# Performance work log

Measured on AMD Instinct MI355X. Metric: run time of the kernel, lower is better.

The kernel has to match this reference:

```python
import jax, jax.numpy as jnp
import numpy as np
import math

DIM = 1024
HEADS = 16
HEAD_DIM = DIM // HEADS
FFN = 4096
B, S = 2, 2048
EPS = 1e-12


def layernorm(x, w, b):
    u = jnp.mean(x, axis=-1, keepdims=True)
    s = jnp.mean((x - u) ** 2, axis=-1, keepdims=True)
    return w * ((x - u) / jnp.sqrt(s + EPS)) + b


def setup_inputs() -> dict:
    key = jax.random.key(0)
    ks = jax.random.split(key, 8)
    scale = 0.02
    return {
        "x": jax.random.normal(ks[0], (B, S, DIM), dtype=jnp.float32),
        "mask": jnp.zeros((1, 1, S, S), dtype=jnp.float32),
        "wq": jax.random.normal(ks[1], (DIM, DIM), dtype=jnp.float32) * scale,
        "wk": jax.random.normal(ks[2], (DIM, DIM), dtype=jnp.float32) * scale,
        "wv": jax.random.normal(ks[3], (DIM, DIM), dtype=jnp.float32) * scale,
        "wo": jax.random.normal(ks[4], (DIM, DIM), dtype=jnp.float32) * scale,
        "w1": jax.random.normal(ks[5], (DIM, FFN), dtype=jnp.float32) * scale,
        "w2": jax.random.normal(ks[6], (FFN, DIM), dtype=jnp.float32) * scale,
        "ln1_w": jnp.ones((DIM,), dtype=jnp.float32),
        "ln1_b": jnp.zeros((DIM,), dtype=jnp.float32),
        "ln2_w": jnp.ones((DIM,), dtype=jnp.float32),
        "ln2_b": jnp.zeros((DIM,), dtype=jnp.float32),
    }


def reference(x, mask, wq, wk, wv, wo, w1, w2, ln1_w, ln1_b, ln2_w, ln2_b):
    # --- attention sub-block (pre-LN) ---
    h = layernorm(x, ln1_w, ln1_b)
    q = (h @ wq).reshape(B, S, HEADS, HEAD_DIM).transpose(0, 2, 1, 3)  # [B,H,S,D]
    k = (h @ wk).reshape(B, S, HEADS, HEAD_DIM).transpose(0, 2, 1, 3)
    v = (h @ wv).reshape(B, S, HEADS, HEAD_DIM).transpose(0, 2, 1, 3)
    scores = jnp.einsum("bhsd,bhtd->bhst", q, k) / math.sqrt(HEAD_DIM)
    scores = scores + mask
    probs = jax.nn.softmax(scores.astype(jnp.float32), axis=-1).astype(q.dtype)
    attn = jnp.einsum("bhst,bhtd->bhsd", probs, v)  # [B,H,S,D]
    attn = attn.transpose(0, 2, 1, 3).reshape(B, S, DIM)
    x = x + attn @ wo
    # --- FFN sub-block (pre-LN) ---
    h = layernorm(x, ln2_w, ln2_b)
    m = jax.nn.gelu(h @ w1, approximate=False) @ w2
    return x + m
```

## Files before the change

kernel.cpp:

```cpp
#include <hip/hip_runtime.h>
#include <math.h>


#define DIMSZ 1024
#define SEQ   2048
#define BATCH 2
#define NHEAD 16
#define HD    64
#define FFNSZ 4096
#define ROWS  (BATCH*SEQ)

typedef __attribute__((ext_vector_type(8))) short bf8_t;
typedef __attribute__((ext_vector_type(4))) float f4_t;

__device__ __forceinline__ unsigned short f2bf(float f) {
  union { float f; unsigned u; } c; c.f = f;
  unsigned u = c.u;
  return (unsigned short)((u + 0x7fffu + ((u >> 16) & 1u)) >> 16);
}

__device__ __forceinline__ float fast_exp2(float x) {
#if __has_builtin(__builtin_amdgcn_exp2f)
  return __builtin_amdgcn_exp2f(x);
#else
  return exp2f(x);
#endif
}

__device__ __forceinline__ unsigned int pk_trunc_bf16(float a, float b) {
#if __has_builtin(__builtin_amdgcn_perm)
  return __builtin_amdgcn_perm(__float_as_uint(b), __float_as_uint(a), 0x07060302u);
#else
  return (__float_as_uint(b) & 0xffff0000u) | (__float_as_uint(a) >> 16);
#endif
}

__device__ __forceinline__ void async16(const void* g, void* l) {
  __builtin_amdgcn_global_load_lds((const __attribute__((address_space(1))) void*)g,
                                   (__attribute__((address_space(3))) void*)l,
                                   16, 0, 0);
}

__device__ __forceinline__ f4_t mfma_bf16(bf8_t a, bf8_t b, f4_t c) {
  return __builtin_amdgcn_mfma_f32_16x16x32_bf16(a, b, c, 0, 0, 0);
}

__global__ __launch_bounds__(256) void ln_kernel(const float* __restrict__ x,
                                                 const float* __restrict__ w,
                                                 const float* __restrict__ b,
                                                 unsigned short* __restrict__ out) {
  int row  = blockIdx.x * 4 + (threadIdx.x >> 6);
  int lane = threadIdx.x & 63;
  const float4* xr = (const float4*)(x + (size_t)row * DIMSZ);
  float4 v[4];
  float s = 0.f, s2 = 0.f;
#pragma unroll
  for (int i = 0; i < 4; ++i) {
    v[i] = xr[lane + 64*i];
    s  += (v[i].x + v[i].y) + (v[i].z + v[i].w);
    s2 += (v[i].x*v[i].x + v[i].y*v[i].y) + (v[i].z*v[i].z + v[i].w*v[i].w);
  }
#pragma unroll
  for (int off = 32; off; off >>= 1) {
    s  += __shfl_xor(s,  off);
    s2 += __shfl_xor(s2, off);
  }
  float mean = s * (1.f/DIMSZ);
  float var  = s2 * (1.f/DIMSZ) - mean*mean;
  float rstd = rsqrtf(var + 1e-12f);
  const float4* wr = (const float4*)w;
  const float4* br = (const float4*)b;
#pragma unroll
  for (int i = 0; i < 4; ++i) {
    float4 wv = wr[lane + 64*i];
    float4 bv = br[lane + 64*i];
    ushort4 o;
    o.x = f2bf((v[i].x - mean) * rstd * wv.x + bv.x);
    o.y = f2bf((v[i].y - mean) * rstd * wv.y + bv.y);
    o.z = f2bf((v[i].z - mean) * rstd * wv.z + bv.z);
    o.w = f2bf((v[i].w - mean) * rstd * wv.w + bv.w);
    *(ushort4*)(out + (size_t)row * DIMSZ + (size_t)(lane + 64*i) * 4) = o;
  }
}

__global__ __launch_bounds__(256) void wtrans4_kernel(const float* __restrict__ w0,
                                                      const float* __restrict__ w1,
                                                      const float* __restrict__ w2,
                                                      const float* __restrict__ w3,
                                                      unsigned short* __restrict__ o0,
                                                      unsigned short* __restrict__ o1,
                                                      unsigned short* __restrict__ o2,
                                                      unsigned short* __restrict__ o3) {
  const int K = 1024, N = 1024;
  const float* w = (blockIdx.z == 0) ? w0 : (blockIdx.z == 1) ? w1 : (blockIdx.z == 2) ? w2 : w3;
  unsigned short* wT = (blockIdx.z == 0) ? o0 : (blockIdx.z == 1) ? o1 : (blockIdx.z == 2) ? o2 : o3;
  __shared__ float t[32][33];
  int tx = threadIdx.x & 31, ty = threadIdx.x >> 5;
  int n0 = blockIdx.x * 32, k0 = blockIdx.y * 32;
#pragma unroll
  for (int i = 0; i < 4; ++i)
    t[ty + 8*i][tx] = w[(size_t)(k0 + ty + 8*i) * N + n0 + tx];
  __syncthreads();
#pragma unroll
  for (int i = 0; i < 4; ++i)
    wT[(size_t)(n0 + ty + 8*i) * K + k0 + tx] = f2bf(t[tx][ty + 8*i]);
}

__global__ __launch_bounds__(256) void wtrans_kernel(const float* __restrict__ w,
                                                     unsigned short* __restrict__ wT,
                                                     int K, int N) {
  __shared__ float t[32][33];
  int tx = threadIdx.x & 31, ty = threadIdx.x >> 5;
  int n0 = blockIdx.x * 32, k0 = blockIdx.y * 32;
#pragma unroll
  for (int i = 0; i < 4; ++i)
    t[ty + 8*i][tx] = w[(size_t)(k0 + ty + 8*i) * N + n0 + tx];
  __syncthreads();
#pragma unroll
  for (int i = 0; i < 4; ++i)
    wT[(size_t)(n0 + ty + 8*i) * K + k0 + tx] = f2bf(t[tx][ty + 8*i]);
}

__global__ __launch_bounds__(256) void vt_kernel(const unsigned short* __restrict__ qkv,
                                                 unsigned short* __restrict__ vt) {
  __shared__ unsigned short tile[64][65];
  int bh = blockIdx.y, b = bh >> 4, h = bh & 15;
  int s0 = blockIdx.x * 64;
  int tx = threadIdx.x & 63, ty = threadIdx.x >> 6;
#pragma unroll
  for (int i = 0; i < 16; ++i) {
    int s = ty + i*4;
    tile[s][tx] = qkv[((size_t)(b*SEQ) + s0 + s) * 3072 + 2048 + h*HD + tx];
  }
  __syncthreads();
#pragma unroll
  for (int i = 0; i < 16; ++i) {
    int d = ty + i*4;
    vt[((size_t)bh * HD + d) * SEQ + s0 + tx] = tile[tx][d];
  }
}

template<int EPI, int NT>
__global__ __launch_bounds__(256) void gemm_bt(const unsigned short* __restrict__ A,
                                               const unsigned short* __restrict__ Bt,
                                               void* __restrict__ Cv,
                                               const float* __restrict__ res,
                                               int M, int N, int K) {
  constexpr int JT = NT / 32;
  __shared__ unsigned short As[2][128][32];
  __shared__ unsigned short Bs[2][NT][32];
  int tid  = threadIdx.x;
  int wv   = tid >> 6, lane = tid & 63, quad = lane >> 4, ml = lane & 15;
  int wrow = (wv >> 1) * 64, wcol = (wv & 1) * (NT/2);
  const unsigned short* Ab = A  + (size_t)blockIdx.y * 128 * K;
  const unsigned short* Bb = Bt + (size_t)blockIdx.x * NT  * K;

  f4_t acc[4][JT];
#pragma unroll
  for (int i = 0; i < 4; ++i)
#pragma unroll
    for (int j = 0; j < JT; ++j) acc[i][j] = (f4_t){0.f, 0.f, 0.f, 0.f};

  int r0 = tid >> 2, c0 = (tid & 3) * 8;

  for (int k0 = 0; k0 < K; k0 += 64) {
#pragma unroll
    for (int h = 0; h < 2; ++h) {
      const unsigned short* ap = Ab + (size_t)r0 * K + k0 + h*32 + c0;
      async16(ap,          &As[h][r0][c0]);
      async16(ap + 64*K,   &As[h][r0 + 64][c0]);
      const unsigned short* bp = Bb + (size_t)r0 * K + k0 + h*32 + c0;
      async16(bp,          &Bs[h][r0][c0]);
      if constexpr (NT == 128)
        async16(bp + 64*K, &Bs[h][r0 + 64][c0]);
    }
    __syncthreads();

#pragma unroll
    for (int h = 0; h < 2; ++h) {
      bf8_t af[4], bfr[JT];
#pragma unroll
      for (int i = 0; i < 4; ++i)
        af[i] = *(const bf8_t*)(&As[h][wrow + i*16 + ml][quad * 8]);
#pragma unroll
      for (int j = 0; j < JT; ++j)
        bfr[j] = *(const bf8_t*)(&Bs[h][wcol + j*16 + ml][quad * 8]);
#pragma unroll
      for (int i = 0; i < 4; ++i)
#pragma unroll
        for (int j = 0; j < JT; ++j)
          acc[i][j] = mfma_bf16(bfr[j], af[i], acc[i][j]);
    }
    __syncthreads();
  }

#pragma unroll
  for (int i = 0; i < 4; ++i) {
    int m = blockIdx.y * 128 + wrow + i*16 + ml;
#pragma unroll
    for (int j = 0; j < JT; ++j) {
      int n = blockIdx.x * NT + wcol + j*16 + quad*4;
      size_t off = (size_t)m * N + n;
      if constexpr (EPI == 2) {
        float4 rv = *(const float4*)(res + off);
        float4 ov;
        ov.x = rv.x + acc[i][j][0];
        ov.y = rv.y + acc[i][j][1];
        ov.z = rv.z + acc[i][j][2];
        ov.w = rv.w + acc[i][j][3];
        *(float4*)((float*)Cv + off) = ov;
      } else {
        float v0 = acc[i][j][0], v1 = acc[i][j][1], v2 = acc[i][j][2], v3 = acc[i][j][3];
        if constexpr (EPI == 1) {
          v0 = 0.5f * v0 * (1.f + erff(v0 * 0.70710678118654752f));
          v1 = 0.5f * v1 * (1.f + erff(v1 * 0.70710678118654752f));
          v2 = 0.5f * v2 * (1.f + erff(v2 * 0.70710678118654752f));
          v3 = 0.5f * v3 * (1.f + erff(v3 * 0.70710678118654752f));
        }
        ushort4 o;
        o.x = f2bf(v0); o.y = f2bf(v1); o.z = f2bf(v2); o.w = f2bf(v3);
        *(ushort4*)((unsigned short*)Cv + off) = o;
      }
    }
  }
}

__global__ __launch_bounds__(256) void attn_kernel(const unsigned short* __restrict__ qkv,
                                                   const unsigned short* __restrict__ vt,
                                                   const float* __restrict__ mask,
                                                   unsigned short* __restrict__ attnout) {
  __shared__ unsigned short Ks[2][64][32];
  __shared__ unsigned short Vs[2][64][32];
  __shared__ unsigned short Ps[4][16][72];

  int bh = blockIdx.y, b = bh >> 4, h = bh & 15;
  int tid = threadIdx.x;
  int wv = tid >> 6, lane = tid & 63;
  int quad = lane >> 4, ml = lane & 15;
  int q0 = blockIdx.x * 64;
  int q  = q0 + wv * 16 + ml;

  const unsigned short* qrow = qkv + ((size_t)(b*SEQ) + q) * 3072 + h*HD;
  bf8_t qf0 = *(const bf8_t*)(qrow + quad*8);
  bf8_t qf1 = *(const bf8_t*)(qrow + 32 + quad*8);

  const unsigned short* kbase = qkv + (size_t)(b*SEQ) * 3072 + DIMSZ + h*HD;
  const unsigned short* vbase = vt + (size_t)bh * HD * SEQ;
  const float* mrow = mask + (size_t)q * SEQ;

  int srow = tid >> 2;
  int scol = (tid & 3) * 8;

  f4_t O[4];
#pragma unroll
  for (int dt = 0; dt < 4; ++dt) O[dt] = (f4_t){0.f, 0.f, 0.f, 0.f};
  float lR = 0.f;

  const float C1 = 0.18033688011112042f;
  const float C2 = 1.4426950408889634f;

  for (int t0 = 0; t0 < SEQ; t0 += 64) {
    float4 mv[4];
#pragma unroll
    for (int mt = 0; mt < 4; ++mt)
      mv[mt] = *(const float4*)(mrow + t0 + mt*16 + quad*4);

    __syncthreads();
#pragma unroll
    for (int dh = 0; dh < 2; ++dh)
      async16(kbase + (size_t)(t0 + srow) * 3072 + dh*32 + scol,
              &Ks[dh][0][0] + (size_t)tid * 8);
#pragma unroll
    for (int kc = 0; kc < 2; ++kc)
      async16(vbase + (size_t)srow * SEQ + t0 + kc*32 + scol,
              &Vs[kc][0][0] + (size_t)tid * 8);
    __syncthreads();

#pragma unroll
    for (int mt = 0; mt < 4; ++mt) {
      bf8_t kf0 = *(const bf8_t*)(&Ks[0][mt*16 + ml][quad*8]);
      bf8_t kf1 = *(const bf8_t*)(&Ks[1][mt*16 + ml][quad*8]);
      f4_t s = (f4_t){0.f, 0.f, 0.f, 0.f};
      s = mfma_bf16(kf0, qf0, s);
      s = mfma_bf16(kf1, qf1, s);
      float p0 = fast_exp2(fmaf(s[0], C1, mv[mt].x * C2));
      float p1 = fast_exp2(fmaf(s[1], C1, mv[mt].y * C2));
      float p2 = fast_exp2(fmaf(s[2], C1, mv[mt].z * C2));
      float p3 = fast_exp2(fmaf(s[3], C1, mv[mt].w * C2));
      lR += (p0 + p1) + (p2 + p3);
      uint2 pk;
      pk.x = pk_trunc_bf16(p0, p1);
      pk.y = pk_trunc_bf16(p2, p3);
      *(uint2*)(&Ps[wv][ml][mt*16 + quad*4]) = pk;
    }

#pragma unroll
    for (int kc = 0; kc < 2; ++kc) {
      bf8_t pf = *(const bf8_t*)(&Ps[wv][ml][kc*32 + quad*8]);
#pragma unroll
      for (int dt = 0; dt < 4; ++dt) {
        bf8_t vf = *(const bf8_t*)(&Vs[kc][dt*16 + ml][quad*8]);
        O[dt] = mfma_bf16(vf, pf, O[dt]);
      }
    }
  }

  lR += __shfl_xor(lR, 16);
  lR += __shfl_xor(lR, 32);
  float linv = 1.f / lR;
#pragma unroll
  for (int dt = 0; dt < 4; ++dt) {
    ushort4 o;
    o.x = f2bf(O[dt][0] * linv);
    o.y = f2bf(O[dt][1] * linv);
    o.z = f2bf(O[dt][2] * linv);
    o.w = f2bf(O[dt][3] * linv);
    *(ushort4*)(attnout + ((size_t)(b*SEQ) + q) * DIMSZ + h*HD + dt*16 + quad*4) = o;
  }
}

extern "C" void kernel_launch(void* const* d_in, const int* in_sizes, int n_in,
                              void* d_out, int out_size, void* d_ws, size_t ws_size,
                              hipStream_t stream) {
  const float* x    = (const float*)d_in[0];
  const float* mask = (const float*)d_in[1];
  const float* wq   = (const float*)d_in[2];
  const float* wk   = (const float*)d_in[3];
  const float* wvp  = (const float*)d_in[4];
  const float* wo   = (const float*)d_in[5];
  const float* w1   = (const float*)d_in[6];
  const float* w2   = (const float*)d_in[7];
  const float* ln1w = (const float*)d_in[8];
  const float* ln1b = (const float*)d_in[9];
  const float* ln2w = (const float*)d_in[10];
  const float* ln2b = (const float*)d_in[11];
  float* out = (float*)d_out;

  char* ws = (char*)d_ws;
  unsigned short* wqkvT  = (unsigned short*)(ws + 0);
  unsigned short* woT    = (unsigned short*)(ws + 6291456);
  unsigned short* w1T    = (unsigned short*)(ws + 8388608);
  unsigned short* w2T    = (unsigned short*)(ws + 16777216);
  unsigned short* attno  = (unsigned short*)(ws + 25165824);
  float*          x2     = (float*)         (ws + 33554432);
  unsigned short* hbuf   = (unsigned short*)(ws + 50331648);
  unsigned short* qkvb   = (unsigned short*)(ws + 58720256);
  unsigned short* vtb    = (unsigned short*)(ws + 83886080);
  unsigned short* gbuf   = (unsigned short*)(ws + 58720256);

  ln_kernel<<<ROWS/4, 256, 0, stream>>>(x, ln1w, ln1b, hbuf);
  wtrans4_kernel<<<dim3(32, 32, 4), 256, 0, stream>>>(wq, wk, wvp, wo,
      wqkvT, wqkvT + 1024*1024, wqkvT + 2*1024*1024, woT);
  wtrans_kernel<<<dim3(128, 32), 256, 0, stream>>>(w1, w1T, 1024, 4096);
  wtrans_kernel<<<dim3(32, 128), 256, 0, stream>>>(w2, w2T, 4096, 1024);
  gemm_bt<0,128><<<dim3(3072/128, 4096/128), 256, 0, stream>>>(hbuf, wqkvT, qkvb, nullptr, ROWS, 3072, 1024);
  vt_kernel<<<dim3(SEQ/64, BATCH*NHEAD), 256, 0, stream>>>(qkvb, vtb);
  attn_kernel<<<dim3(SEQ/64, BATCH*NHEAD), 256, 0, stream>>>(qkvb, vtb, mask, attno);
  gemm_bt<2,64><<<dim3(1024/64, 4096/128), 256, 0, stream>>>(attno, woT, x2, x, ROWS, 1024, 1024);
  ln_kernel<<<ROWS/4, 256, 0, stream>>>(x2, ln2w, ln2b, hbuf);
  gemm_bt<1,128><<<dim3(4096/128, 4096/128), 256, 0, stream>>>(hbuf, w1T, gbuf, nullptr, ROWS, FFNSZ, 1024);
  gemm_bt<2,64><<<dim3(1024/64, 4096/128), 256, 0, stream>>>(gbuf, w2T, out, x2, ROWS, 1024, 4096);

  (void)in_sizes; (void)n_in; (void)out_size; (void)ws_size;
}
```

Measured before the change: 424.1 us.

## Split attention over the key dimension and merge partial results in a combine kernel

The attention kernel is split along the key axis into two halves, doubling the number of blocks. Each half writes unnormalized partial outputs in bf16 and its partial row sums to workspace. A new combine kernel adds the two partials, divides by the total sum and writes the final attention output. This is meant to raise parallelism and shorten each block's serial key loop, at the cost of extra global traffic, a second launch, and bf16 rounding of the partial outputs. The simple summed merge relies on the existing softmax using a fixed scale rather than a running max.

```diff
diff --git a/kernel.cpp b/kernel.cpp
--- a/kernel.cpp
+++ b/kernel.cpp
@@ -9,6 +9,8 @@
 #define HD    64
 #define FFNSZ 4096
 #define ROWS  (BATCH*SEQ)
+#define KSPLIT 2
+#define KRANGE (SEQ/KSPLIT)
 
 typedef __attribute__((ext_vector_type(8))) short bf8_t;
 typedef __attribute__((ext_vector_type(4))) float f4_t;
@@ -17,6 +19,10 @@
   union { float f; unsigned u; } c; c.f = f;
   unsigned u = c.u;
   return (unsigned short)((u + 0x7fffu + ((u >> 16) & 1u)) >> 16);
+}
+
+__device__ __forceinline__ float bf2f(unsigned short u) {
+  union { unsigned u; float f; } c; c.u = ((unsigned)u) << 16; return c.f;
 }
 
 __device__ __forceinline__ float fast_exp2(float x) {
@@ -225,28 +231,31 @@
   }
 }
 
-__global__ __launch_bounds__(256) void attn_kernel(const unsigned short* __restrict__ qkv,
-                                                   const unsigned short* __restrict__ vt,
-                                                   const float* __restrict__ mask,
-                                                   unsigned short* __restrict__ attnout) {
+__global__ __launch_bounds__(256) void attn_part(const unsigned short* __restrict__ qkv,
+                                                 const unsigned short* __restrict__ vt,
+                                                 const float* __restrict__ mask,
+                                                 unsigned short* __restrict__ pbuf,
+                                                 float* __restrict__ lbuf) {
   __shared__ unsigned short Ks[2][64][32];
   __shared__ unsigned short Vs[2][64][32];
   __shared__ unsigned short Ps[4][16][72];
 
-  int bh = blockIdx.y, b = bh >> 4, h = bh & 15;
+  int kz = blockIdx.y;
+  int bh = blockIdx.z, b = bh >> 4, h = bh & 15;
   int tid = threadIdx.x;
   int wv = tid >> 6, lane = tid & 63;
   int quad = lane >> 4, ml = lane & 15;
   int q0 = blockIdx.x * 64;
   int q  = q0 + wv * 16 + ml;
+  int kbeg = kz * KRANGE;
 
   const unsigned short* qrow = qkv + ((size_t)(b*SEQ) + q) * 3072 + h*HD;
   bf8_t qf0 = *(const bf8_t*)(qrow + quad*8);
   bf8_t qf1 = *(const bf8_t*)(qrow + 32 + quad*8);
 
-  const unsigned short* kbase = qkv + (size_t)(b*SEQ) * 3072 + DIMSZ + h*HD;
-  const unsigned short* vbase = vt + (size_t)bh * HD * SEQ;
-  const float* mrow = mask + (size_t)q * SEQ;
+  const unsigned short* kbase = qkv + ((size_t)(b*SEQ) + kbeg) * 3072 + DIMSZ + h*HD;
+  const unsigned short* vbase = vt + (size_t)bh * HD * SEQ + kbeg;
+  const float* mrow = mask + (size_t)q * SEQ + kbeg;
 
   int srow = tid >> 2;
   int scol = (tid & 3) * 8;
@@ -259,7 +268,7 @@
   const float C1 = 0.18033688011112042f;
   const float C2 = 1.4426950408889634f;
 
-  for (int t0 = 0; t0 < SEQ; t0 += 64) {
+  for (int t0 = 0; t0 < KRANGE; t0 += 64) {
     float4 mv[4];
 #pragma unroll
     for (int mt = 0; mt < 4; ++mt)
@@ -307,16 +316,41 @@
 
   lR += __shfl_xor(lR, 16);
   lR += __shfl_xor(lR, 32);
-  float linv = 1.f / lR;
+  size_t pb = ((size_t)(bh * KSPLIT + kz) * SEQ + q) * HD;
 #pragma unroll
   for (int dt = 0; dt < 4; ++dt) {
     ushort4 o;
-    o.x = f2bf(O[dt][0] * linv);
-    o.y = f2bf(O[dt][1] * linv);
-    o.z = f2bf(O[dt][2] * linv);
-    o.w = f2bf(O[dt][3] * linv);
-    *(ushort4*)(attnout + ((size_t)(b*SEQ) + q) * DIMSZ + h*HD + dt*16 + quad*4) = o;
-  }
+    o.x = f2bf(O[dt][0]);
+    o.y = f2bf(O[dt][1]);
+    o.z = f2bf(O[dt][2]);
+    o.w = f2bf(O[dt][3]);
+    *(ushort4*)(pbuf + pb + dt*16 + quad*4) = o;
+  }
+  if (quad == 0)
+    lbuf[(size_t)(bh * KSPLIT + kz) * SEQ + q] = lR;
+}
+
+__global__ __launch_bounds__(256) void attn_combine(const unsigned short* __restrict__ pbuf,
+                                                    const float* __restrict__ lbuf,
+                                                    unsigned short* __restrict__ attno) {
+  int t = blockIdx.x * 256 + threadIdx.x;
+  int dchunk = t & 15;
+  int q = (t >> 4) & (SEQ - 1);
+  int bh = t >> 15;
+  int b = bh >> 4, h = bh & 15;
+  size_t o0 = ((size_t)(bh * KSPLIT + 0) * SEQ + q) * HD + dchunk * 4;
+  size_t o1 = ((size_t)(bh * KSPLIT + 1) * SEQ + q) * HD + dchunk * 4;
+  ushort4 a = *(const ushort4*)(pbuf + o0);
+  ushort4 c = *(const ushort4*)(pbuf + o1);
+  float l = lbuf[(size_t)(bh * KSPLIT + 0) * SEQ + q]
+          + lbuf[(size_t)(bh * KSPLIT + 1) * SEQ + q];
+  float inv = 1.f / l;
+  ushort4 o;
+  o.x = f2bf((bf2f(a.x) + bf2f(c.x)) * inv);
+  o.y = f2bf((bf2f(a.y) + bf2f(c.y)) * inv);
+  o.z = f2bf((bf2f(a.z) + bf2f(c.z)) * inv);
+  o.w = f2bf((bf2f(a.w) + bf2f(c.w)) * inv);
+  *(ushort4*)(attno + ((size_t)(b*SEQ) + q) * DIMSZ + h*HD + dchunk*4) = o;
 }
 
 extern "C" void kernel_launch(void* const* d_in, const int* in_sizes, int n_in,
@@ -347,6 +381,8 @@
   unsigned short* qkvb   = (unsigned short*)(ws + 58720256);
   unsigned short* vtb    = (unsigned short*)(ws + 83886080);
   unsigned short* gbuf   = (unsigned short*)(ws + 58720256);
+  unsigned short* pbuf   = (unsigned short*)(ws + 33554432);
+  float*          lbuf   = (float*)         (ws + 50331648);
 
   ln_kernel<<<ROWS/4, 256, 0, stream>>>(x, ln1w, ln1b, hbuf);
   wtrans4_kernel<<<dim3(32, 32, 4), 256, 0, stream>>>(wq, wk, wvp, wo,
@@ -355,7 +391,8 @@
   wtrans_kernel<<<dim3(32, 128), 256, 0, stream>>>(w2, w2T, 4096, 1024);
   gemm_bt<0,128><<<dim3(3072/128, 4096/128), 256, 0, stream>>>(hbuf, wqkvT, qkvb, nullptr, ROWS, 3072, 1024);
   vt_kernel<<<dim3(SEQ/64, BATCH*NHEAD), 256, 0, stream>>>(qkvb, vtb);
-  attn_kernel<<<dim3(SEQ/64, BATCH*NHEAD), 256, 0, stream>>>(qkvb, vtb, mask, attno);
+  attn_part<<<dim3(SEQ/64, KSPLIT, BATCH*NHEAD), 256, 0, stream>>>(qkvb, vtb, mask, pbuf, lbuf);
+  attn_combine<<<(BATCH*NHEAD*SEQ*(HD/4))/256, 256, 0, stream>>>(pbuf, lbuf, attno);
   gemm_bt<2,64><<<dim3(1024/64, 4096/128), 256, 0, stream>>>(attno, woT, x2, x, ROWS, 1024, 1024);
   ln_kernel<<<ROWS/4, 256, 0, stream>>>(x2, ln2w, ln2b, hbuf);
   gemm_bt<1,128><<<dim3(4096/128, 4096/128), 256, 0, stream>>>(hbuf, w1T, gbuf, nullptr, ROWS, FFNSZ, 1024);
```

Result: no change. 423.9 us (-0.0%).
